# Kernel tuning notes

Hardware: AMD Instinct MI355X
Metric: run time of the kernel (lower is better)

## Reference

```python
import jax, jax.numpy as jnp
import numpy as np

B, S, E, A = 64, 1024, 512, 128


def setup_inputs() -> dict:
    key = jax.random.key(0)
    ks = jax.random.split(key, 12)
    sc = 0.02
    states = jax.random.normal(ks[0], (B, S, E), jnp.float32)
    cls_token = jax.random.normal(ks[1], (B, E), jnp.float32)
    # ragged lengths in [2, S]; force at least one full-length row so padded width == S-1
    lengths = jax.random.randint(ks[2], (B,), 2, S + 1).at[0].set(S).astype(jnp.int32)
    position_action = (jax.random.randint(ks[3], (B,), 0, S) % (lengths - 1)).astype(jnp.int32)
    symbol_action = jax.random.randint(ks[4], (B,), 0, A).astype(jnp.int32)
    W1p = jax.random.normal(ks[5], (2 * E, 2 * E), jnp.float32) * sc
    b1p = jnp.zeros((2 * E,), jnp.float32)
    w2p = jax.random.normal(ks[6], (2 * E,), jnp.float32) * sc
    b2p = jnp.zeros((1,), jnp.float32)
    W1s = jax.random.normal(ks[7], (2 * E, 2 * E), jnp.float32) * sc
    b1s = jnp.zeros((2 * E,), jnp.float32)
    W2s = jax.random.normal(ks[8], (2 * E, A), jnp.float32) * sc
    b2s = jnp.zeros((A,), jnp.float32)
    Wc1 = jax.random.normal(ks[9], (E, E), jnp.float32) * sc
    bc1 = jnp.zeros((E,), jnp.float32)
    wc2 = jax.random.normal(ks[10], (E,), jnp.float32) * sc
    bc2 = jnp.zeros((1,), jnp.float32)
    return dict(states=states, cls_token=cls_token, W1p=W1p, b1p=b1p, w2p=w2p, b2p=b2p,
                W1s=W1s, b1s=b1s, W2s=W2s, b2s=b2s, Wc1=Wc1, bc1=bc1, wc2=wc2, bc2=bc2,
                lengths=lengths, position_action=position_action, symbol_action=symbol_action)


def reference(states, cls_token, W1p, b1p, w2p, b2p, W1s, b1s, W2s, b2s,
              Wc1, bc1, wc2, bc2, lengths, position_action, symbol_action):
    b, s, e = states.shape
    # --- get_adjacent_pairs + position_actor MLP, fused (no [.,2E] concat materialized) ---
    first, second = states[:, :-1], states[:, 1:]            # (B, S-1, E) each
    h = jax.nn.relu(jnp.einsum('bse,ef->bsf', first, W1p[:e])
                    + jnp.einsum('bse,ef->bsf', second, W1p[e:]) + b1p)  # (B, S-1, 2E)
    scores = jnp.einsum('bsf,f->bs', h, w2p) + b2p            # (B, S-1)
    # --- map_scores_to_sentences: pad invalid pair slots with -inf ---
    pos_mask = jnp.arange(s - 1)[None, :] < (lengths - 1)[:, None]
    scores = jnp.where(pos_mask, scores, -jnp.inf)
    logp = jax.nn.log_softmax(scores, axis=1)
    logp_pos = jnp.take_along_axis(logp, position_action[:, None], axis=1)[:, 0]
    logp_m = jnp.where(pos_mask, logp, 0.0)                   # safe for -inf slots
    ent_pos = -jnp.sum(jnp.exp(logp) * logp_m, axis=1)
    # --- symbol head on the pair embedding at the chosen split position ---
    bidx = jnp.arange(b)
    e1 = states[bidx, position_action]                        # (B, E)
    e2 = states[bidx, position_action + 1]                    # (B, E)
    sh = jax.nn.relu(e1 @ W1s[:e] + e2 @ W1s[e:] + b1s)       # (B, 2E)
    slogp = jax.nn.log_softmax(sh @ W2s + b2s, axis=1)        # (B, A)
    logp_sym = jnp.take_along_axis(slogp, symbol_action[:, None], axis=1)[:, 0]
    ent_sym = -jnp.sum(jnp.exp(slogp) * slogp, axis=1)
    # --- critic on cls token ---
    val = jax.nn.relu(cls_token @ Wc1 + bc1) @ wc2 + bc2      # (B,)
    return jnp.stack([logp_pos, logp_sym, val, ent_pos, ent_sym], axis=0)  # (5, B)
```

## Files before the change

### kernel.cpp

```cpp
#include <hip/hip_runtime.h>
#include <stdint.h>

#define BDIM 64
#define SDIM 1024
#define EDIM 512
#define ADIM 128
#define M_ROWS (BDIM*(SDIM-1))
#define KDIM 1024
#define NDIM 1024

typedef unsigned short u16;
typedef __attribute__((ext_vector_type(8))) short short8;
typedef __attribute__((ext_vector_type(4))) float floatx4;
typedef const __attribute__((address_space(1))) void as1_void;
typedef __attribute__((address_space(3))) void as3_void;

__device__ inline u16 f2bf(float f){
  unsigned int u = __float_as_uint(f);
  u += 0x7fffu + ((u >> 16) & 1u);
  return (u16)(u >> 16);
}

__global__ __launch_bounds__(1024) void k_prep(
    const float* __restrict__ states, const float* __restrict__ cls,
    const float* __restrict__ W1p, const float* __restrict__ W1s,
    const float* __restrict__ b1s, const float* __restrict__ Wc1,
    const float* __restrict__ bc1, const float* __restrict__ wc2,
    const float* __restrict__ bc2, const int* __restrict__ lengths,
    const int* __restrict__ pos_action,
    u16* __restrict__ sbf, u16* __restrict__ wt,
    float* __restrict__ sh, int* __restrict__ live_list,
    float* __restrict__ out)
{
  __shared__ float smem[64*65];
  const int blk = blockIdx.x, tid = threadIdx.x;

  if (blk < 1024){
    int i = blk*1024 + tid;
#pragma unroll
    for (int it = 0; it < 4; ++it, i += 1048576){
      int row = i >> 6;
      int s = row & 1023, b = row >> 10;
      if (s < lengths[b]){
        const float4* sp = (const float4*)states + (size_t)i*2;
        float4 a = sp[0], c = sp[1];
        short8 v;
        v[0]=(short)f2bf(a.x); v[1]=(short)f2bf(a.y); v[2]=(short)f2bf(a.z); v[3]=(short)f2bf(a.w);
        v[4]=(short)f2bf(c.x); v[5]=(short)f2bf(c.y); v[6]=(short)f2bf(c.z); v[7]=(short)f2bf(c.w);
        ((short8*)sbf)[i] = v;
      }
    }
    return;
  }
  if (blk < 1280){
    float (*tile)[65] = (float(*)[65])smem;
    int tb = blk - 1024;
    int k0 = (tb & 15)*64, n0 = (tb >> 4)*64;
    int tx = tid & 63, ty = tid >> 6;
    for (int j = ty; j < 64; j += 16) tile[j][tx] = W1p[(size_t)(k0+j)*NDIM + n0 + tx];
    __syncthreads();
    for (int j = ty; j < 64; j += 16) wt[(size_t)(n0+j)*KDIM + k0 + tx] = f2bf(tile[tx][j]);
    return;
  }
  if (blk == 1280){
    int* flags = (int*)smem;
    if (tid < 512){
      int m_start = tid*128;
      int m_end = m_start + 127; if (m_end > M_ROWS-1) m_end = M_ROWS-1;
      int b0 = m_start / 1023, b1 = m_end / 1023;
      flags[tid] = !(b0 == b1 && (m_start - b0*1023) >= lengths[b0]-1);
    }
    __syncthreads();
    if (tid == 0){
      int c = 0;
      for (int i2 = 0; i2 < 512; ++i2) if (flags[i2]) live_list[c++] = i2;
      live_list[512] = c;
    }
    return;
  }
  if (blk < 1537){
    float* xs  = smem;
    float* red = smem + 1024;
    int rb = blk - 1281;
    int b = rb >> 2, n0 = (rb & 3)*256;
    int pa = pos_action[b];
    const float* src = states + (size_t)(b*SDIM + pa) * EDIM;
    xs[tid] = src[tid];
    __syncthreads();
    int n = n0 + (tid & 255);
    int k0 = (tid >> 8) * 256;
    float acc = 0.f;
#pragma unroll 8
    for (int jj = 0; jj < 256; ++jj){
      int k = k0 + jj;
      acc = fmaf(xs[k], W1s[(size_t)k*1024 + n], acc);
    }
    red[tid] = acc;
    __syncthreads();
    if (tid < 256){
      float s = red[tid] + red[tid+256] + red[tid+512] + red[tid+768];
      sh[b*1024 + n0 + tid] = fmaxf(s + b1s[n0 + tid], 0.f);
    }
    return;
  }
  {
    float* xs  = smem;
    float* red = smem + 512;
    float* r2  = smem + 1536;
    int b = blk - 1537;
    if (tid < 512) xs[tid] = cls[b*EDIM + tid];
    __syncthreads();
    int n = tid & 511;
    int k0 = (tid >> 9) * 256;
    float acc = 0.f;
#pragma unroll 8
    for (int jj = 0; jj < 256; ++jj){
      int k = k0 + jj;
      acc = fmaf(xs[k], Wc1[(size_t)k*EDIM + n], acc);
    }
    red[tid] = acc;
    __syncthreads();
    float p = 0.f;
    if (tid < 512){
      float h = red[tid] + red[tid + 512];
      p = fmaxf(h + bc1[tid], 0.f) * wc2[tid];
    }
    for (int off = 32; off; off >>= 1) p += __shfl_xor(p, off);
    if ((tid & 63) == 0) r2[tid >> 6] = p;
    __syncthreads();
    if (tid == 0){
      float s = bc2[0];
#pragma unroll
      for (int jj = 0; jj < 16; ++jj) s += r2[jj];
      out[128 + b] = s;
    }
  }
}

__global__ __launch_bounds__(256, 2) void k_gemm_scores(
    const u16* __restrict__ sbf, const u16* __restrict__ wt,
    const float* __restrict__ b1p, const float* __restrict__ w2p,
    const int* __restrict__ live_list, float* __restrict__ scores_p)
{
  __shared__ short8 Ash[1024];
  __shared__ short8 Bsh[1024];
  __shared__ float comb[2][128];
  const int tid = threadIdx.x;
  const int w = tid >> 6, l = tid & 63;
  const int j = blockIdx.x;
  const int tl = ((j >> 6) << 3) | (j & 7);
  const int nt = (j >> 3) & 7;
  if (tl >= live_list[512]) return;
  const int mt = live_list[tl];

  const int lrow8 = l >> 3;
  const int c = (l & 7) ^ lrow8;
  const char* sbase = (const char*)sbf;
  const char* wbase = (const char*)wt;
  int offA[4], offB[4];
#pragma unroll
  for (int i = 0; i < 4; ++i){
    int mloc = (w*4 + i)*8 + lrow8;
    int mg = mt*128 + mloc;
    if (mg >= M_ROWS) mg = 0;
    int bb = mg / 1023;
    int ss = mg - bb*1023;
    offA[i] = bb*1048576 + ss*1024 + c*16;
    int nloc = (w*4 + i)*8 + lrow8;
    offB[i] = (nt*128 + nloc)*2048 + c*16;
  }

  const int r = l & 15, q = l >> 4;
  const int wm = w & 1, wn = w >> 1;
  int aIdx[4], bIdx[4];
#pragma unroll
  for (int i = 0; i < 4; ++i){
    int m = wm*64 + i*16 + r;
    aIdx[i] = m*8 + (q ^ (r & 7));
    int n = wn*64 + i*16 + r;
    bIdx[i] = n*8 + (q ^ (r & 7));
  }

  floatx4 acc[4][4];
#pragma unroll
  for (int a = 0; a < 4; ++a)
#pragma unroll
    for (int b = 0; b < 4; ++b) acc[a][b] = (floatx4)(0.0f);

  for (int step = 0; step < 16; ++step){
    const int ktb = step * 128;
    __syncthreads();
#pragma unroll
    for (int i = 0; i < 4; ++i){
      __builtin_amdgcn_global_load_lds((as1_void*)(sbase + offA[i] + ktb),
                                       (as3_void*)((char*)Ash + (w*4 + i)*1024), 16, 0, 0);
    }
#pragma unroll
    for (int i = 0; i < 4; ++i){
      __builtin_amdgcn_global_load_lds((as1_void*)(wbase + offB[i] + ktb),
                                       (as3_void*)((char*)Bsh + (w*4 + i)*1024), 16, 0, 0);
    }
    __syncthreads();
#pragma unroll
    for (int kh = 0; kh < 2; ++kh){
      short8 af[4], bf[4];
#pragma unroll
      for (int i = 0; i < 4; ++i) af[i] = Ash[aIdx[i] ^ (kh*4)];
#pragma unroll
      for (int i = 0; i < 4; ++i) bf[i] = Bsh[bIdx[i] ^ (kh*4)];
#pragma unroll
      for (int mi = 0; mi < 4; ++mi)
#pragma unroll
        for (int ni = 0; ni < 4; ++ni)
          acc[mi][ni] = __builtin_amdgcn_mfma_f32_16x16x32_bf16(af[mi], bf[ni], acc[mi][ni], 0, 0, 0);
    }
  }

  const int mrow0 = mt*128 + wm*64;
  const int ncol0 = nt*128 + wn*64;
  float* dst = scores_p + (nt << 16);
#pragma unroll
  for (int mi = 0; mi < 4; ++mi){
    float t0 = 0.f, t1 = 0.f, t2 = 0.f, t3 = 0.f;
#pragma unroll
    for (int ni = 0; ni < 4; ++ni){
      int n = ncol0 + ni*16 + r;
      float bb = b1p[n], ww = w2p[n];
      floatx4 a = acc[mi][ni];
      t0 += fmaxf(a[0] + bb, 0.f) * ww;
      t1 += fmaxf(a[1] + bb, 0.f) * ww;
      t2 += fmaxf(a[2] + bb, 0.f) * ww;
      t3 += fmaxf(a[3] + bb, 0.f) * ww;
    }
#pragma unroll
    for (int off = 1; off < 16; off <<= 1){
      t0 += __shfl_xor(t0, off);
      t1 += __shfl_xor(t1, off);
      t2 += __shfl_xor(t2, off);
      t3 += __shfl_xor(t3, off);
    }
    int lrow = mi*16 + q*4;
    if (wn == 0 && r == 0){
      comb[wm][lrow+0] = t0; comb[wm][lrow+1] = t1;
      comb[wm][lrow+2] = t2; comb[wm][lrow+3] = t3;
    }
    __syncthreads();
    if (wn == 1 && r == 0){
      int row = mrow0 + lrow;
      float4 v4 = make_float4(t0 + comb[wm][lrow+0], t1 + comb[wm][lrow+1],
                              t2 + comb[wm][lrow+2], t3 + comb[wm][lrow+3]);
      if (row + 3 < M_ROWS) *(float4*)(dst + row) = v4;
      else {
        if (row   < M_ROWS) dst[row]   = v4.x;
        if (row+1 < M_ROWS) dst[row+1] = v4.y;
        if (row+2 < M_ROWS) dst[row+2] = v4.z;
      }
    }
    __syncthreads();
  }
}

__global__ __launch_bounds__(1024) void k_post(
    const float* __restrict__ scores_p, const float* __restrict__ sh,
    const float* __restrict__ W2s, const float* __restrict__ b2s,
    const int* __restrict__ lengths, const int* __restrict__ pos_action,
    const int* __restrict__ sym_action, float* __restrict__ out)
{
  __shared__ float smem[2208];
  const int blk = blockIdx.x, tid = threadIdx.x;
  if (blk < 64){
    float* sc   = smem;
    float* red  = smem + 1024;
    float* red2 = smem + 1040;
    int b = blk;
    int L = lengths[b] - 1;
    const float* sp = scores_p + b*1023;
    float mx = -1e30f;
    for (int s = tid; s < L; s += 1024){
      float v = 0.f;
#pragma unroll
      for (int ntI = 0; ntI < 8; ++ntI) v += sp[(ntI << 16) + s];
      sc[s] = v;
      mx = fmaxf(mx, v);
    }
    for (int off = 32; off; off >>= 1) mx = fmaxf(mx, __shfl_xor(mx, off));
    if ((tid & 63) == 0) red[tid >> 6] = mx;
    __syncthreads();
    mx = -1e30f;
#pragma unroll
    for (int jj = 0; jj < 16; ++jj) mx = fmaxf(mx, red[jj]);
    float se = 0.f, ses = 0.f;
    for (int s = tid; s < L; s += 1024){
      float v = sc[s];
      float e = expf(v - mx);
      se += e; ses += e * v;
    }
    for (int off = 32; off; off >>= 1){ se += __shfl_xor(se, off); ses += __shfl_xor(ses, off); }
    __syncthreads();
    if ((tid & 63) == 0){ red[tid >> 6] = se; red2[tid >> 6] = ses; }
    __syncthreads();
    if (tid == 0){
      float S = 0.f, SS = 0.f;
#pragma unroll
      for (int jj = 0; jj < 16; ++jj){ S += red[jj]; SS += red2[jj]; }
      float logZ = logf(S);
      int pa = pos_action[b];
      out[b]       = sc[pa] - mx - logZ;
      out[192 + b] = mx + logZ - SS / S;
    }
    return;
  }
  {
    float* xs  = smem;
    float* red = smem + 1024;
    float* lg  = smem + 2048;
    float* r2  = smem + 2176;
    float* r3  = smem + 2192;
    int b = blk - 64;
    xs[tid] = sh[b*1024 + tid];
    __syncthreads();
    int n = tid & 127;
    int f0 = (tid >> 7) * 128;
    float acc = 0.f;
#pragma unroll 8
    for (int jj = 0; jj < 128; ++jj){
      int f = f0 + jj;
      acc = fmaf(xs[f], W2s[(size_t)f*ADIM + n], acc);
    }
    red[tid] = acc;
    __syncthreads();
    if (tid < 128){
      float s = b2s[tid];
#pragma unroll
      for (int jj = 0; jj < 8; ++jj) s += red[tid + jj*128];
      lg[tid] = s;
    }
    __syncthreads();
    float v = (tid < 128) ? lg[tid] : -1e30f;
    float mx = v;
    for (int off = 32; off; off >>= 1) mx = fmaxf(mx, __shfl_xor(mx, off));
    if ((tid & 63) == 0) r2[tid >> 6] = mx;
    __syncthreads();
    mx = -1e30f;
#pragma unroll
    for (int jj = 0; jj < 16; ++jj) mx = fmaxf(mx, r2[jj]);
    float e = (tid < 128) ? expf(v - mx) : 0.f;
    float se = e, ses = (tid < 128) ? e * v : 0.f;
    for (int off = 32; off; off >>= 1){ se += __shfl_xor(se, off); ses += __shfl_xor(ses, off); }
    __syncthreads();
    if ((tid & 63) == 0){ r2[tid >> 6] = se; r3[tid >> 6] = ses; }
    __syncthreads();
    if (tid == 0){
      float S = 0.f, SS = 0.f;
#pragma unroll
      for (int jj = 0; jj < 16; ++jj){ S += r2[jj]; SS += r3[jj]; }
      float logZ = logf(S);
      out[64 + b]  = lg[sym_action[b]] - mx - logZ;
      out[256 + b] = mx + logZ - SS / S;
    }
  }
}

extern "C" void kernel_launch(void* const* d_in, const int* in_sizes, int n_in,
                              void* d_out, int out_size, void* d_ws, size_t ws_size,
                              hipStream_t stream){
  const float* states = (const float*)d_in[0];
  const float* cls    = (const float*)d_in[1];
  const float* W1p    = (const float*)d_in[2];
  const float* b1p    = (const float*)d_in[3];
  const float* w2p    = (const float*)d_in[4];
  const float* W1s    = (const float*)d_in[6];
  const float* b1s    = (const float*)d_in[7];
  const float* W2s    = (const float*)d_in[8];
  const float* b2s    = (const float*)d_in[9];
  const float* Wc1    = (const float*)d_in[10];
  const float* bc1    = (const float*)d_in[11];
  const float* wc2    = (const float*)d_in[12];
  const float* bc2    = (const float*)d_in[13];
  const int* lengths  = (const int*)d_in[14];
  const int* pos_a    = (const int*)d_in[15];
  const int* sym_a    = (const int*)d_in[16];
  float* out = (float*)d_out;

  char* ws = (char*)d_ws;
  u16* sbf        = (u16*)ws;
  u16* wt         = (u16*)(ws + 67108864);
  float* scores_p = (float*)(ws + 69206016);
  float* sh       = (float*)(ws + 71303168);
  int* live       = (int*)(ws + 71565312);

  k_prep<<<1601, 1024, 0, stream>>>(states, cls, W1p, W1s, b1s, Wc1, bc1, wc2, bc2,
                                    lengths, pos_a, sbf, wt, sh, live, out);
  k_gemm_scores<<<4096, 256, 0, stream>>>(sbf, wt, b1p, w2p, live, scores_p);
  k_post<<<128, 1024, 0, stream>>>(scores_p, sh, W2s, b2s, lengths, pos_a, sym_a, out);
}
```

Baseline: 337.0 us.

## Compact valid pair rows into dense list and accumulate scores with atomics

Replaces the per-128-row-tile liveness list with a prefix-sum compaction, so that only valid (b, s) pair rows are packed densely into GEMM M-tiles through a row-index gather. Partially padded tiles no longer waste MFMA work. Per-N-tile partial scores are now combined with float atomicAdd into a single zeroed buffer instead of eight partial arrays plus an LDS combine with barriers. The costs are a serial prefix scan in one block, atomic contention (8 N-tiles per row), and nondeterministic summation order.

```diff
diff --git a/kernel.cpp b/kernel.cpp
--- a/kernel.cpp
+++ b/kernel.cpp
@@ -29,8 +29,8 @@
     const float* __restrict__ bc2, const int* __restrict__ lengths,
     const int* __restrict__ pos_action,
     u16* __restrict__ sbf, u16* __restrict__ wt,
-    float* __restrict__ sh, int* __restrict__ live_list,
-    float* __restrict__ out)
+    float* __restrict__ sh, int* __restrict__ rows, int* __restrict__ aux,
+    float* __restrict__ scores, float* __restrict__ out)
 {
   __shared__ float smem[64*65];
   const int blk = blockIdx.x, tid = threadIdx.x;
@@ -55,6 +55,8 @@
   if (blk < 1280){
     float (*tile)[65] = (float(*)[65])smem;
     int tb = blk - 1024;
+    int zi = tb*1024 + tid;
+    if (zi < 65536) scores[zi] = 0.f;
     int k0 = (tb & 15)*64, n0 = (tb >> 4)*64;
     int tx = tid & 63, ty = tid >> 6;
     for (int j = ty; j < 64; j += 16) tile[j][tx] = W1p[(size_t)(k0+j)*NDIM + n0 + tx];
@@ -63,18 +65,21 @@
     return;
   }
   if (blk == 1280){
-    int* flags = (int*)smem;
-    if (tid < 512){
-      int m_start = tid*128;
-      int m_end = m_start + 127; if (m_end > M_ROWS-1) m_end = M_ROWS-1;
-      int b0 = m_start / 1023, b1 = m_end / 1023;
-      flags[tid] = !(b0 == b1 && (m_start - b0*1023) >= lengths[b0]-1);
-    }
-    __syncthreads();
+    __shared__ int scum[65];
     if (tid == 0){
       int c = 0;
-      for (int i2 = 0; i2 < 512; ++i2) if (flags[i2]) live_list[c++] = i2;
-      live_list[512] = c;
+      for (int b = 0; b < 64; ++b){ scum[b] = c; c += lengths[b] - 1; }
+      scum[64] = c;
+    }
+    __syncthreads();
+    if (tid < 65) aux[tid] = scum[tid];
+    if (tid == 0){
+      aux[70] = scum[64];
+      aux[71] = (scum[64] + 127) >> 7;
+    }
+    for (int b = 0; b < 64; ++b){
+      int base = scum[b], L = scum[b+1] - scum[b];
+      for (int i2 = tid; i2 < L; i2 += 1024) rows[base + i2] = (b << 10) + i2;
     }
     return;
   }
@@ -140,18 +145,18 @@
 __global__ __launch_bounds__(256, 2) void k_gemm_scores(
     const u16* __restrict__ sbf, const u16* __restrict__ wt,
     const float* __restrict__ b1p, const float* __restrict__ w2p,
-    const int* __restrict__ live_list, float* __restrict__ scores_p)
+    const int* __restrict__ rows, const int* __restrict__ aux,
+    float* __restrict__ scores)
 {
   __shared__ short8 Ash[1024];
   __shared__ short8 Bsh[1024];
-  __shared__ float comb[2][128];
   const int tid = threadIdx.x;
   const int w = tid >> 6, l = tid & 63;
   const int j = blockIdx.x;
   const int tl = ((j >> 6) << 3) | (j & 7);
   const int nt = (j >> 3) & 7;
-  if (tl >= live_list[512]) return;
-  const int mt = live_list[tl];
+  const int total = aux[70];
+  if (tl >= aux[71]) return;
 
   const int lrow8 = l >> 3;
   const int c = (l & 7) ^ lrow8;
@@ -161,11 +166,10 @@
 #pragma unroll
   for (int i = 0; i < 4; ++i){
     int mloc = (w*4 + i)*8 + lrow8;
-    int mg = mt*128 + mloc;
-    if (mg >= M_ROWS) mg = 0;
-    int bb = mg / 1023;
-    int ss = mg - bb*1023;
-    offA[i] = bb*1048576 + ss*1024 + c*16;
+    int mg = tl*128 + mloc;
+    if (mg >= total) mg = 0;
+    int rs = rows[mg];
+    offA[i] = rs*1024 + c*16;
     int nloc = (w*4 + i)*8 + lrow8;
     offB[i] = (nt*128 + nloc)*2048 + c*16;
   }
@@ -216,9 +220,8 @@
     }
   }
 
-  const int mrow0 = mt*128 + wm*64;
+  const int mrow0 = tl*128 + wm*64;
   const int ncol0 = nt*128 + wn*64;
-  float* dst = scores_p + (nt << 16);
 #pragma unroll
   for (int mi = 0; mi < 4; ++mi){
     float t0 = 0.f, t1 = 0.f, t2 = 0.f, t3 = 0.f;
@@ -239,32 +242,22 @@
       t2 += __shfl_xor(t2, off);
       t3 += __shfl_xor(t3, off);
     }
-    int lrow = mi*16 + q*4;
-    if (wn == 0 && r == 0){
-      comb[wm][lrow+0] = t0; comb[wm][lrow+1] = t1;
-      comb[wm][lrow+2] = t2; comb[wm][lrow+3] = t3;
-    }
-    __syncthreads();
-    if (wn == 1 && r == 0){
-      int row = mrow0 + lrow;
-      float4 v4 = make_float4(t0 + comb[wm][lrow+0], t1 + comb[wm][lrow+1],
-                              t2 + comb[wm][lrow+2], t3 + comb[wm][lrow+3]);
-      if (row + 3 < M_ROWS) *(float4*)(dst + row) = v4;
-      else {
-        if (row   < M_ROWS) dst[row]   = v4.x;
-        if (row+1 < M_ROWS) dst[row+1] = v4.y;
-        if (row+2 < M_ROWS) dst[row+2] = v4.z;
-      }
-    }
-    __syncthreads();
+    if (r == 0){
+      int row = mrow0 + mi*16 + q*4;
+      if (row + 0 < total) atomicAdd(&scores[row + 0], t0);
+      if (row + 1 < total) atomicAdd(&scores[row + 1], t1);
+      if (row + 2 < total) atomicAdd(&scores[row + 2], t2);
+      if (row + 3 < total) atomicAdd(&scores[row + 3], t3);
+    }
   }
 }
 
 __global__ __launch_bounds__(1024) void k_post(
-    const float* __restrict__ scores_p, const float* __restrict__ sh,
+    const float* __restrict__ scores, const float* __restrict__ sh,
     const float* __restrict__ W2s, const float* __restrict__ b2s,
-    const int* __restrict__ lengths, const int* __restrict__ pos_action,
-    const int* __restrict__ sym_action, float* __restrict__ out)
+    const int* __restrict__ aux, const int* __restrict__ lengths,
+    const int* __restrict__ pos_action, const int* __restrict__ sym_action,
+    float* __restrict__ out)
 {
   __shared__ float smem[2208];
   const int blk = blockIdx.x, tid = threadIdx.x;
@@ -274,12 +267,10 @@
     float* red2 = smem + 1040;
     int b = blk;
     int L = lengths[b] - 1;
-    const float* sp = scores_p + b*1023;
+    const float* sp = scores + aux[b];
     float mx = -1e30f;
     for (int s = tid; s < L; s += 1024){
-      float v = 0.f;
-#pragma unroll
-      for (int ntI = 0; ntI < 8; ++ntI) v += sp[(ntI << 16) + s];
+      float v = sp[s];
       sc[s] = v;
       mx = fmaxf(mx, v);
     }
@@ -383,14 +374,15 @@
   float* out = (float*)d_out;
 
   char* ws = (char*)d_ws;
-  u16* sbf        = (u16*)ws;
-  u16* wt         = (u16*)(ws + 67108864);
-  float* scores_p = (float*)(ws + 69206016);
-  float* sh       = (float*)(ws + 71303168);
-  int* live       = (int*)(ws + 71565312);
+  u16* sbf      = (u16*)ws;
+  u16* wt       = (u16*)(ws + 67108864);
+  float* scores = (float*)(ws + 69206016);
+  float* sh     = (float*)(ws + 69468160);
+  int* rows     = (int*)(ws + 69730304);
+  int* aux      = (int*)(ws + 69992448);
 
   k_prep<<<1601, 1024, 0, stream>>>(states, cls, W1p, W1s, b1s, Wc1, bc1, wc2, bc2,
-                                    lengths, pos_a, sbf, wt, sh, live, out);
-  k_gemm_scores<<<4096, 256, 0, stream>>>(sbf, wt, b1p, w2p, live, scores_p);
-  k_post<<<128, 1024, 0, stream>>>(scores_p, sh, W2s, b2s, lengths, pos_a, sym_a, out);
-}
+                                    lengths, pos_a, sbf, wt, sh, rows, aux, scores, out);
+  k_gemm_scores<<<4096, 256, 0, stream>>>(sbf, wt, b1p, w2p, rows, aux, scores);
+  k_post<<<128, 1024, 0, stream>>>(scores, sh, W2s, b2s, aux, lengths, pos_a, sym_a, out);
+}
```

New measurement: 321.6 us, median of 2. 1.05x faster.
